# Kernel optimization log

Hardware: AMD Instinct MI355X
Metric: run time of the kernel (lower is better)

Reference implementation:

```python
import jax, jax.numpy as jnp
import numpy as np

N_NODES = 50000
N_EDGES = 600000
IN_DIM, HID_DIM, OUT_DIM = 128, 256, 40


def setup_inputs() -> dict:
    key = jax.random.key(0)
    ks = jax.random.split(key, 10)
    x = jax.random.normal(ks[0], (N_NODES, IN_DIM), dtype=jnp.float32)
    edge_index = jax.random.randint(ks[1], (2, N_EDGES), 0, N_NODES, dtype=jnp.int64)
    def lin(k, out_d, in_d):
        s = 1.0 / np.sqrt(in_d)
        return jax.random.uniform(k, (out_d, in_d), jnp.float32, -s, s)
    # SAGEConv: lin_l (on aggregated neighbors, with bias) + lin_r (on self, no bias)
    params = {
        "Wl1": lin(ks[2], HID_DIM, IN_DIM), "bl1": jnp.zeros((HID_DIM,), jnp.float32), "Wr1": lin(ks[3], HID_DIM, IN_DIM),
        "Wl2": lin(ks[4], HID_DIM, HID_DIM), "bl2": jnp.zeros((HID_DIM,), jnp.float32), "Wr2": lin(ks[5], HID_DIM, HID_DIM),
        "Wl3": lin(ks[6], OUT_DIM, HID_DIM), "bl3": jnp.zeros((OUT_DIM,), jnp.float32), "Wr3": lin(ks[7], OUT_DIM, HID_DIM),
    }
    return {"x": x, "edge_index": edge_index, **params}


def _sage_conv(x, src, dst, Wl, bl, Wr):
    # mean-aggregate source features into destination nodes
    n = x.shape[0]
    agg = jax.ops.segment_sum(x[src], dst, num_segments=n)          # [N, d_in]
    cnt = jax.ops.segment_sum(jnp.ones_like(dst, dtype=x.dtype), dst, num_segments=n)
    mean = agg / jnp.maximum(cnt, 1.0)[:, None]
    return mean @ Wl.T + bl + x @ Wr.T


def reference(x, edge_index, Wl1, bl1, Wr1, Wl2, bl2, Wr2, Wl3, bl3, Wr3):
    src, dst = edge_index[0], edge_index[1]
    h = _sage_conv(x, src, dst, Wl1, bl1, Wr1)
    h = jax.nn.relu(h)  # dropout is identity in eval mode
    h = _sage_conv(h, src, dst, Wl2, bl2, Wr2)
    h = jax.nn.relu(h)
    h = _sage_conv(h, src, dst, Wl3, bl3, Wr3)
    return jax.nn.log_softmax(h, axis=1)
```

## Files before the change

### kernel.cpp

```cpp
#include <hip/hip_runtime.h>
#include <hip/hip_bf16.h>

#define IN_DIM 128
#define HID_DIM 256
#define OUT_DIM 40
#define SCAN_CHUNK 2048

typedef __attribute__((ext_vector_type(8))) __bf16 bf16x8;
typedef __attribute__((ext_vector_type(4))) float f32x4;

__device__ inline ushort f2bf(float f) {
    uint u = __builtin_bit_cast(uint, f);
    u = (u + 0x7fff + ((u >> 16) & 1)) >> 16;
    return (ushort)u;
}
__device__ inline float bfl(uint u) { return __builtin_bit_cast(float, u << 16); }
__device__ inline float bfh(uint u) { return __builtin_bit_cast(float, u & 0xffff0000u); }

__device__ inline void gload_lds16(const ushort* g, ushort* l) {
    __builtin_amdgcn_global_load_lds((const __attribute__((address_space(1))) void*)g,
                                     (__attribute__((address_space(3))) void*)l, 16, 0, 0);
}

__device__ inline int xcd_swizzle(int b, int G) {
    int q = G >> 3, r = G & 7;
    int xcd = b & 7, j = b >> 3;
    return (xcd < r ? xcd * (q + 1) : r * (q + 1) + (xcd - r) * q) + j;
}

__global__ __launch_bounds__(256) void prep_kernel(
    const float* __restrict__ x, ushort* __restrict__ xb, int n4, int XB,
    const float* __restrict__ Wl1, const float* __restrict__ Wr1,
    const float* __restrict__ Wl2, const float* __restrict__ Wr2,
    const float* __restrict__ Wl3, const float* __restrict__ Wr3,
    ushort* __restrict__ o1l, ushort* __restrict__ o1r,
    ushort* __restrict__ o2l, ushort* __restrict__ o2r,
    ushort* __restrict__ o3l, ushort* __restrict__ o3r, int WB,
    const int* __restrict__ dst, int* __restrict__ cnt, int E) {
    int b = blockIdx.x;
    if (b < XB) {
        int i = b * 256 + threadIdx.x;
        if (i < n4) {
            float4 v = ((const float4*)x)[i];
            uint2 o;
            o.x = (uint)f2bf(v.x) | ((uint)f2bf(v.y) << 16);
            o.y = (uint)f2bf(v.z) | ((uint)f2bf(v.w) << 16);
            ((uint2*)xb)[i] = o;
        }
        return;
    }
    b -= XB;
    if (b < WB) {
        int idx = b * 256 + threadIdx.x;
        if (idx < 32768) {
            int j = idx & 7, ln = (idx >> 3) & 15, quad = (idx >> 7) & 3;
            int kk = (idx >> 9) & 3, ct = (idx >> 11) & 3, cb = idx >> 13;
            int o = cb * 64 + ct * 16 + ln;
            int k = kk * 32 + quad * 8 + j;
            o1l[idx] = f2bf(Wl1[o * 128 + k]);
            o1r[idx] = f2bf(Wr1[o * 128 + k]);
            return;
        }
        idx -= 32768;
        if (idx < 65536) {
            int j = idx & 7, ln = (idx >> 3) & 15, quad = (idx >> 7) & 3;
            int kk = (idx >> 9) & 7, ct = (idx >> 12) & 3, cb = idx >> 14;
            int o = cb * 64 + ct * 16 + ln;
            int k = kk * 32 + quad * 8 + j;
            o2l[idx] = f2bf(Wl2[o * 256 + k]);
            o2r[idx] = f2bf(Wr2[o * 256 + k]);
            return;
        }
        idx -= 65536;
        if (idx < 48 * 256) {
            int row = idx >> 8;
            int col = idx & 255;
            ushort vl = 0, vr = 0;
            if (row < OUT_DIM) {
                vl = f2bf(Wl3[row * 256 + col]);
                vr = f2bf(Wr3[row * 256 + col]);
            }
            o3l[idx] = vl;
            o3r[idx] = vr;
        }
        return;
    }
    b -= WB;
    int e = b * 256 + threadIdx.x;
    if (e < E) atomicAdd(&cnt[dst[e]], 1);
}

__global__ __launch_bounds__(256) void scan_pass1(const int* __restrict__ cnt,
                                                  int* __restrict__ bsum, int N) {
    __shared__ int red[256];
    const int base = blockIdx.x * SCAN_CHUNK;
    int s = 0;
    for (int i = threadIdx.x; i < SCAN_CHUNK; i += 256) {
        int idx = base + i;
        if (idx < N) s += cnt[idx];
    }
    red[threadIdx.x] = s;
    __syncthreads();
    for (int o = 128; o > 0; o >>= 1) {
        if (threadIdx.x < o) red[threadIdx.x] += red[threadIdx.x + o];
        __syncthreads();
    }
    if (threadIdx.x == 0) bsum[blockIdx.x] = red[0];
}

__global__ __launch_bounds__(256) void scan_pass3(const int* __restrict__ cnt,
                                                  const int* __restrict__ bsum,
                                                  int* __restrict__ rowptr,
                                                  int* __restrict__ cursor,
                                                  float* __restrict__ inv,
                                                  int N, int E, int SB) {
    __shared__ int ls[256];
    __shared__ int boff;
    if (threadIdx.x == 0) {
        int r = 0;
        for (int i = 0; i < blockIdx.x; ++i) r += bsum[i];
        boff = r;
    }
    const int tbase = blockIdx.x * SCAN_CHUNK + threadIdx.x * 8;
    int c[8];
    int s = 0;
#pragma unroll
    for (int j = 0; j < 8; ++j) {
        int idx = tbase + j;
        c[j] = (idx < N) ? cnt[idx] : 0;
        s += c[j];
    }
    ls[threadIdx.x] = s;
    __syncthreads();
    for (int o = 1; o < 256; o <<= 1) {
        int u = (threadIdx.x >= o) ? ls[threadIdx.x - o] : 0;
        __syncthreads();
        ls[threadIdx.x] += u;
        __syncthreads();
    }
    int run = boff + ls[threadIdx.x] - s;
#pragma unroll
    for (int j = 0; j < 8; ++j) {
        int idx = tbase + j;
        if (idx < N) {
            rowptr[idx] = run;
            cursor[idx] = run;
            inv[idx] = 1.0f / fmaxf((float)c[j], 1.0f);
            run += c[j];
        }
    }
    if (blockIdx.x == 0 && threadIdx.x == 0) rowptr[N] = E;
}

__global__ __launch_bounds__(256) void fill_kernel(const int* __restrict__ src,
                                                   const int* __restrict__ dst,
                                                   int* __restrict__ cursor,
                                                   int* __restrict__ srcs, int E) {
    int e = blockIdx.x * 256 + threadIdx.x;
    if (e < E) {
        int pos = atomicAdd(&cursor[dst[e]], 1);
        srcs[pos] = src[e];
    }
}

template <int D>
__global__ __launch_bounds__(256) void gather_mean_bf(const ushort* __restrict__ feat,
                                                      const int* __restrict__ rowptr,
                                                      const int* __restrict__ srcs,
                                                      const float* __restrict__ inv,
                                                      ushort* __restrict__ out, int N) {
    constexpr int LPN = D / 8;
    constexpr int NPW = 64 / LPN;
    constexpr int NPB = 4 * NPW;
    const int wave = threadIdx.x >> 6;
    const int lane = threadIdx.x & 63;
    const int sub = lane / LPN;
    const int sl = lane % LPN;
    const int n = blockIdx.x * NPB + wave * NPW + sub;
    const bool alive = n < N;
    const int beg = alive ? rowptr[n] : 0;
    const int end = alive ? rowptr[n + 1] : 0;
    const int col = sl * 8;

    float a0 = 0.f, a1 = 0.f, a2 = 0.f, a3 = 0.f;
    float a4 = 0.f, a5 = 0.f, a6 = 0.f, a7 = 0.f;
    int e = beg;
    for (; e + 3 < end; e += 4) {
        uint4 q[4];
#pragma unroll
        for (int j = 0; j < 4; ++j)
            q[j] = *(const uint4*)&feat[(long long)srcs[e + j] * D + col];
#pragma unroll
        for (int j = 0; j < 4; ++j) {
            a0 += bfl(q[j].x); a1 += bfh(q[j].x);
            a2 += bfl(q[j].y); a3 += bfh(q[j].y);
            a4 += bfl(q[j].z); a5 += bfh(q[j].z);
            a6 += bfl(q[j].w); a7 += bfh(q[j].w);
        }
    }
    for (; e < end; ++e) {
        uint4 q = *(const uint4*)&feat[(long long)srcs[e] * D + col];
        a0 += bfl(q.x); a1 += bfh(q.x);
        a2 += bfl(q.y); a3 += bfh(q.y);
        a4 += bfl(q.z); a5 += bfh(q.z);
        a6 += bfl(q.w); a7 += bfh(q.w);
    }
    if (alive) {
        const float sc = inv[n];
        uint4 o;
        o.x = (uint)f2bf(a0 * sc) | ((uint)f2bf(a1 * sc) << 16);
        o.y = (uint)f2bf(a2 * sc) | ((uint)f2bf(a3 * sc) << 16);
        o.z = (uint)f2bf(a4 * sc) | ((uint)f2bf(a5 * sc) << 16);
        o.w = (uint)f2bf(a6 * sc) | ((uint)f2bf(a7 * sc) << 16);
        *(uint4*)&out[(long long)n * D + col] = o;
    }
}

template <int K, bool RELU, bool OUTBF>
__global__ __launch_bounds__(512, 2) void sage_gemm_mfma(const ushort* __restrict__ Amean,
                                                         const ushort* __restrict__ Aself,
                                                         const ushort* __restrict__ Wl,
                                                         const float* __restrict__ bias,
                                                         const ushort* __restrict__ Wr,
                                                         void* __restrict__ outv, int N, int O,
                                                         int G) {
    constexpr int NK = K / 32;
    constexpr int TILE2 = 128 * K;
    constexpr int CHUNKS = TILE2 / 512;
    __shared__ __align__(16) ushort Ws[TILE2];

    const int tid = threadIdx.x;
    const int wave = tid >> 6;
    const int lane = tid & 63;
    const int ln = lane & 15;
    const int quad = lane >> 4;

    const int wid = xcd_swizzle(blockIdx.x, G);
    const int c2 = wid & 1;
    const int bm0 = (wid >> 1) * 256;

    int arow[2];
#pragma unroll
    for (int rt = 0; rt < 2; ++rt) {
        int r = bm0 + wave * 32 + rt * 16 + ln;
        arow[rt] = min(r, N - 1);
    }

    f32x4 acc[2][8] = {};

#pragma unroll
    for (int p = 0; p < 2; ++p) {
        const ushort* __restrict__ A = p ? Aself : Amean;
        const ushort* __restrict__ gsrc = (p ? Wr : Wl) + (size_t)c2 * TILE2;

        if (p) __syncthreads();
#pragma unroll
        for (int c = wave; c < CHUNKS; c += 8)
            gload_lds16(gsrc + c * 512 + lane * 8, &Ws[c * 512]);

        bf16x8 areg[NK][2];
#pragma unroll
        for (int kk = 0; kk < NK; ++kk)
#pragma unroll
            for (int rt = 0; rt < 2; ++rt)
                areg[kk][rt] = *(const bf16x8*)&A[(long long)arow[rt] * K + kk * 32 + quad * 8];

        __syncthreads();

#pragma unroll
        for (int kk = 0; kk < NK; ++kk) {
#pragma unroll
            for (int ct = 0; ct < 8; ++ct) {
                bf16x8 b = *(const bf16x8*)&Ws[((ct * NK + kk) * 64 + lane) * 8];
#pragma unroll
                for (int rt = 0; rt < 2; ++rt)
                    acc[rt][ct] = __builtin_amdgcn_mfma_f32_16x16x32_bf16(areg[kk][rt], b, acc[rt][ct], 0, 0, 0);
            }
        }
    }

#pragma unroll
    for (int rt = 0; rt < 2; ++rt) {
        int rbase = bm0 + wave * 32 + rt * 16 + quad * 4;
#pragma unroll
        for (int ct = 0; ct < 8; ++ct) {
            int col = c2 * 128 + ct * 16 + ln;
            if (col >= O) continue;
            float bv = bias[col];
#pragma unroll
            for (int r = 0; r < 4; ++r) {
                int row = rbase + r;
                if (row >= N) continue;
                float v = acc[rt][ct][r] + bv;
                if (RELU) v = fmaxf(v, 0.f);
                if (OUTBF)
                    ((ushort*)outv)[(long long)row * O + col] = f2bf(v);
                else
                    ((float*)outv)[(long long)row * O + col] = v;
            }
        }
    }
}

template <int K>
__global__ __launch_bounds__(256, 3) void sage_gemm_pre(const ushort* __restrict__ A0,
                                                        const ushort* __restrict__ Wl,
                                                        const ushort* __restrict__ Wr,
                                                        ushort* __restrict__ P,
                                                        float* __restrict__ S, int N, int O) {
    constexpr int KP = 2 * K + 8;
    constexpr int NK = K / 32;
    __shared__ __align__(16) ushort Ws[48 * KP];

    const int tid = threadIdx.x;
    const int wave = tid >> 6;
    const int lane = tid & 63;
    const int ln = lane & 15;
    const int quad = lane >> 4;
    const int bm0 = blockIdx.x * 64;

    const int arow = min(bm0 + wave * 16 + ln, N - 1);

#pragma unroll
    for (int i = tid; i < 48 * (K / 8); i += 256) {
        int row = i / (K / 8);
        int c8 = (i % (K / 8)) * 8;
        *(ulonglong2*)&Ws[row * KP + c8] =
            *(const ulonglong2*)&Wl[(long long)row * K + c8];
        *(ulonglong2*)&Ws[row * KP + K + c8] =
            *(const ulonglong2*)&Wr[(long long)row * K + c8];
    }
    __syncthreads();

#pragma unroll
    for (int phase = 0; phase < 2; ++phase) {
        f32x4 acc[3] = {};
#pragma unroll
        for (int kk = 0; kk < NK; ++kk) {
            bf16x8 a = *(const bf16x8*)&A0[(long long)arow * K + kk * 32 + quad * 8];
#pragma unroll
            for (int ct = 0; ct < 3; ++ct) {
                bf16x8 b = *(const bf16x8*)&Ws[(ct * 16 + ln) * KP + phase * K + kk * 32 + quad * 8];
                acc[ct] = __builtin_amdgcn_mfma_f32_16x16x32_bf16(a, b, acc[ct], 0, 0, 0);
            }
        }
        int rbase = bm0 + wave * 16 + quad * 4;
#pragma unroll
        for (int ct = 0; ct < 3; ++ct) {
            int col = ct * 16 + ln;
            if (col >= O) continue;
#pragma unroll
            for (int r = 0; r < 4; ++r) {
                int row = rbase + r;
                if (row >= N) continue;
                if (phase == 0)
                    P[(long long)row * O + col] = f2bf(acc[ct][r]);
                else
                    S[(long long)row * O + col] = acc[ct][r];
            }
        }
    }
}

__global__ __launch_bounds__(256) void agg_bias_lsm(const ushort* __restrict__ P,
                                                    const float* __restrict__ S,
                                                    const float* __restrict__ bias,
                                                    const int* __restrict__ rowptr,
                                                    const int* __restrict__ srcs,
                                                    const float* __restrict__ inv,
                                                    float* __restrict__ out, int N) {
    const int wave = threadIdx.x >> 6;
    const int lane = threadIdx.x & 63;
    const int n = blockIdx.x * 4 + wave;
    if (n >= N) return;
    const int beg = rowptr[n];
    const int end = rowptr[n + 1];
    const bool act = lane < OUT_DIM;
    const int cidx = act ? lane : 0;

    float acc = 0.f;
    int e = beg;
    for (; e + 3 < end; e += 4) {
        int s0 = srcs[e], s1 = srcs[e + 1], s2 = srcs[e + 2], s3 = srcs[e + 3];
        float v0 = __builtin_bit_cast(float, (uint)P[(long long)s0 * OUT_DIM + cidx] << 16);
        float v1 = __builtin_bit_cast(float, (uint)P[(long long)s1 * OUT_DIM + cidx] << 16);
        float v2 = __builtin_bit_cast(float, (uint)P[(long long)s2 * OUT_DIM + cidx] << 16);
        float v3 = __builtin_bit_cast(float, (uint)P[(long long)s3 * OUT_DIM + cidx] << 16);
        acc += (v0 + v1) + (v2 + v3);
    }
    for (; e < end; ++e)
        acc += __builtin_bit_cast(float, (uint)P[(long long)srcs[e] * OUT_DIM + cidx] << 16);

    float v = act ? (acc * inv[n] + S[(long long)n * OUT_DIM + lane] + bias[lane]) : -INFINITY;
    float m = v;
#pragma unroll
    for (int o = 32; o > 0; o >>= 1) m = fmaxf(m, __shfl_xor(m, o, 64));
    float ex = act ? expf(v - m) : 0.f;
    float sm = ex;
#pragma unroll
    for (int o = 32; o > 0; o >>= 1) sm += __shfl_xor(sm, o, 64);
    float ls = logf(sm);
    if (act) out[(long long)n * OUT_DIM + lane] = v - m - ls;
}

extern "C" void kernel_launch(void* const* d_in, const int* in_sizes, int n_in,
                              void* d_out, int out_size, void* d_ws, size_t ws_size,
                              hipStream_t stream) {
    const float* x   = (const float*)d_in[0];
    const int*   ei  = (const int*)d_in[1];
    const float* Wl1 = (const float*)d_in[2];
    const float* bl1 = (const float*)d_in[3];
    const float* Wr1 = (const float*)d_in[4];
    const float* Wl2 = (const float*)d_in[5];
    const float* bl2 = (const float*)d_in[6];
    const float* Wr2 = (const float*)d_in[7];
    const float* Wl3 = (const float*)d_in[8];
    const float* bl3 = (const float*)d_in[9];
    const float* Wr3 = (const float*)d_in[10];
    float* out = (float*)d_out;

    const int N = in_sizes[0] / IN_DIM;
    const int E = in_sizes[1] / 2;
    const int* src = ei;
    const int* dst = ei + E;

    char* w = (char*)d_ws;
    size_t off = 0;
    auto alloc = [&](size_t bytes) {
        void* p = w + off;
        off = (off + bytes + 255) & ~(size_t)255;
        return p;
    };
    ushort* xb   = (ushort*)alloc((size_t)N * IN_DIM * 2);
    ushort* M    = (ushort*)alloc((size_t)N * HID_DIM * 2);
    ushort* H1   = (ushort*)alloc((size_t)N * HID_DIM * 2);
    ushort* H2   = (ushort*)alloc((size_t)N * HID_DIM * 2);
    ushort* P3   = (ushort*)alloc((size_t)N * OUT_DIM * 2);
    float*  S3   = (float*)alloc((size_t)N * OUT_DIM * 4);
    float*  inv  = (float*)alloc((size_t)N * 4);
    int*    cnt  = (int*)alloc((size_t)N * 4);
    int*    rowptr = (int*)alloc((size_t)(N + 1) * 4);
    int*    cursor = (int*)alloc((size_t)N * 4);
    int*    srcs = (int*)alloc((size_t)E * 4);
    int*    bsum = (int*)alloc(256 * 4);
    ushort* Wl1b = (ushort*)alloc(256 * 128 * 2);
    ushort* Wr1b = (ushort*)alloc(256 * 128 * 2);
    ushort* Wl2b = (ushort*)alloc(256 * 256 * 2);
    ushort* Wr2b = (ushort*)alloc(256 * 256 * 2);
    ushort* Wl3b = (ushort*)alloc(48 * 256 * 2);
    ushort* Wr3b = (ushort*)alloc(48 * 256 * 2);

    const int n4 = N * IN_DIM / 4;
    const int XB = (n4 + 255) / 256;
    const int WB = (32768 + 65536 + 48 * 256 + 255) / 256;
    const int HB = (E + 255) / 256;
    hipMemsetAsync(cnt, 0, (size_t)N * sizeof(int), stream);
    prep_kernel<<<XB + WB + HB, 256, 0, stream>>>(
        x, xb, n4, XB,
        Wl1, Wr1, Wl2, Wr2, Wl3, Wr3,
        Wl1b, Wr1b, Wl2b, Wr2b, Wl3b, Wr3b, WB,
        dst, cnt, E);

    const int SB = (N + SCAN_CHUNK - 1) / SCAN_CHUNK;
    scan_pass1<<<SB, 256, 0, stream>>>(cnt, bsum, N);
    scan_pass3<<<SB, 256, 0, stream>>>(cnt, bsum, rowptr, cursor, inv, N, E, SB);
    fill_kernel<<<HB, 256, 0, stream>>>(src, dst, cursor, srcs, E);

    const int gm = (N + 255) / 256;
    const int G = 2 * gm;
    const int gg128 = (N + 15) / 16;
    const int gg256 = (N + 7) / 8;
    const int gg = (N + 3) / 4;

    gather_mean_bf<IN_DIM><<<gg128, 256, 0, stream>>>(xb, rowptr, srcs, inv, M, N);
    sage_gemm_mfma<IN_DIM, true, true><<<G, 512, 0, stream>>>(
        M, xb, Wl1b, bl1, Wr1b, H1, N, HID_DIM, G);

    gather_mean_bf<HID_DIM><<<gg256, 256, 0, stream>>>(H1, rowptr, srcs, inv, M, N);
    sage_gemm_mfma<HID_DIM, true, true><<<G, 512, 0, stream>>>(
        M, H1, Wl2b, bl2, Wr2b, H2, N, HID_DIM, G);

    sage_gemm_pre<HID_DIM><<<(N + 63) / 64, 256, 0, stream>>>(
        H2, Wl3b, Wr3b, P3, S3, N, OUT_DIM);
    agg_bias_lsm<<<gg, 256, 0, stream>>>(P3, S3, bl3, rowptr, srcs, inv, out, N);
}
```

Before: 341.9 us.

## Stage A tiles in swizzled LDS and halve GEMM row tile to 128

The SAGE GEMM kernel now copies its 128-row activation tile into LDS with direct global-to-LDS loads and an XOR swizzle against bank conflicts, instead of each wave loading its A fragments into registers. The row tile shrinks from 256 to 128, so each wave computes one 16-row strip with 8 accumulators and the grid doubles. Launch bounds rise to 4 blocks per SM to lift occupancy. In exchange, LDS use per block grows (up to 128 KB for K=256, which may limit occupancy) and weights are reloaded for twice as many blocks. An extra 64 KB of scratch is also allocated, apparently as padding for the loads that run past the last row.

```diff
diff --git a/kernel.cpp b/kernel.cpp
--- a/kernel.cpp
+++ b/kernel.cpp
@@ -217,17 +217,21 @@
 }
 
 template <int K, bool RELU, bool OUTBF>
-__global__ __launch_bounds__(512, 2) void sage_gemm_mfma(const ushort* __restrict__ Amean,
+__global__ __launch_bounds__(512, 4) void sage_gemm_mfma(const ushort* __restrict__ Amean,
                                                          const ushort* __restrict__ Aself,
                                                          const ushort* __restrict__ Wl,
                                                          const float* __restrict__ bias,
                                                          const ushort* __restrict__ Wr,
                                                          void* __restrict__ outv, int N, int O,
                                                          int G) {
-    constexpr int NK = K / 32;
-    constexpr int TILE2 = 128 * K;
-    constexpr int CHUNKS = TILE2 / 512;
-    __shared__ __align__(16) ushort Ws[TILE2];
+    constexpr int NKK = K / 32;
+    constexpr int RB = 2 * K;
+    constexpr int LOGRB = (K == 256) ? 9 : 8;
+    constexpr int TILE64 = 64 * K;
+    constexpr int AC = (128 * RB) / 1024;
+    constexpr int WC = (2 * TILE64 * 2) / 1024;
+    __shared__ __align__(16) ushort As[128 * K];
+    __shared__ __align__(16) ushort Wsh[2 * TILE64];
 
     const int tid = threadIdx.x;
     const int wave = tid >> 6;
@@ -237,51 +241,46 @@
 
     const int wid = xcd_swizzle(blockIdx.x, G);
     const int c2 = wid & 1;
-    const int bm0 = (wid >> 1) * 256;
-
-    int arow[2];
-#pragma unroll
-    for (int rt = 0; rt < 2; ++rt) {
-        int r = bm0 + wave * 32 + rt * 16 + ln;
-        arow[rt] = min(r, N - 1);
-    }
-
-    f32x4 acc[2][8] = {};
+    const int bm0 = (wid >> 1) * 128;
+
+    f32x4 acc[8] = {};
 
 #pragma unroll
     for (int p = 0; p < 2; ++p) {
-        const ushort* __restrict__ A = p ? Aself : Amean;
-        const ushort* __restrict__ gsrc = (p ? Wr : Wl) + (size_t)c2 * TILE2;
+        const ushort* __restrict__ A = (p ? Aself : Amean) + (size_t)bm0 * K;
+        const ushort* __restrict__ Wg = (p ? Wr : Wl) + (size_t)c2 * 2 * TILE64;
 
         if (p) __syncthreads();
-#pragma unroll
-        for (int c = wave; c < CHUNKS; c += 8)
-            gload_lds16(gsrc + c * 512 + lane * 8, &Ws[c * 512]);
-
-        bf16x8 areg[NK][2];
-#pragma unroll
-        for (int kk = 0; kk < NK; ++kk)
-#pragma unroll
-            for (int rt = 0; rt < 2; ++rt)
-                areg[kk][rt] = *(const bf16x8*)&A[(long long)arow[rt] * K + kk * 32 + quad * 8];
+
+#pragma unroll
+        for (int c = wave; c < WC; c += 8)
+            gload_lds16(Wg + c * 512 + lane * 8, &Wsh[c * 512]);
+
+#pragma unroll
+        for (int c = wave; c < AC; c += 8) {
+            int q = c * 1024 + lane * 16;
+            int row = q >> LOGRB;
+            int inrow = q & (RB - 1);
+            int srcb = (row << LOGRB) + (inrow ^ ((row & 7) << 4));
+            gload_lds16(A + (srcb >> 1), &As[c * 512]);
+        }
 
         __syncthreads();
 
 #pragma unroll
-        for (int kk = 0; kk < NK; ++kk) {
+        for (int kk = 0; kk < NKK; ++kk) {
+            bf16x8 a = *(const bf16x8*)&As[((wave * 16 + ln) * RB +
+                                            ((kk * 64 + quad * 16) ^ ((ln & 7) << 4))) >> 1];
 #pragma unroll
             for (int ct = 0; ct < 8; ++ct) {
-                bf16x8 b = *(const bf16x8*)&Ws[((ct * NK + kk) * 64 + lane) * 8];
-#pragma unroll
-                for (int rt = 0; rt < 2; ++rt)
-                    acc[rt][ct] = __builtin_amdgcn_mfma_f32_16x16x32_bf16(areg[kk][rt], b, acc[rt][ct], 0, 0, 0);
+                bf16x8 b = *(const bf16x8*)&Wsh[(ct >> 2) * TILE64 + (((ct & 3) * NKK + kk) * 64 + lane) * 8];
+                acc[ct] = __builtin_amdgcn_mfma_f32_16x16x32_bf16(a, b, acc[ct], 0, 0, 0);
             }
         }
     }
 
-#pragma unroll
-    for (int rt = 0; rt < 2; ++rt) {
-        int rbase = bm0 + wave * 32 + rt * 16 + quad * 4;
+    {
+        int rbase = bm0 + wave * 16 + quad * 4;
 #pragma unroll
         for (int ct = 0; ct < 8; ++ct) {
             int col = c2 * 128 + ct * 16 + ln;
@@ -291,7 +290,7 @@
             for (int r = 0; r < 4; ++r) {
                 int row = rbase + r;
                 if (row >= N) continue;
-                float v = acc[rt][ct][r] + bv;
+                float v = acc[ct][r] + bv;
                 if (RELU) v = fmaxf(v, 0.f);
                 if (OUTBF)
                     ((ushort*)outv)[(long long)row * O + col] = f2bf(v);
@@ -449,6 +448,7 @@
     ushort* Wr2b = (ushort*)alloc(256 * 256 * 2);
     ushort* Wl3b = (ushort*)alloc(48 * 256 * 2);
     ushort* Wr3b = (ushort*)alloc(48 * 256 * 2);
+    (void)alloc(64 * 1024);
 
     const int n4 = N * IN_DIM / 4;
     const int XB = (n4 + 255) / 256;
@@ -466,8 +466,8 @@
     scan_pass3<<<SB, 256, 0, stream>>>(cnt, bsum, rowptr, cursor, inv, N, E, SB);
     fill_kernel<<<HB, 256, 0, stream>>>(src, dst, cursor, srcs, E);
 
-    const int gm = (N + 255) / 256;
-    const int G = 2 * gm;
+    const int gmr = (N + 127) / 128;
+    const int G = 2 * gmr;
     const int gg128 = (N + 15) / 16;
     const int gg256 = (N + 7) / 8;
     const int gg = (N + 3) / 4;
```

Measured after the change: 339.6 us. Within noise of the previous version (-0.7%).
